# Performance work log

Hardware: AMD Instinct MI355X
Metric: run time of the kernel (lower is better)

Reference implementation:

```python
import jax, jax.numpy as jnp
import numpy as np

EPS = 0.5
GAM1 = 1.0
GAM2 = 1.0
GAM3 = 1.0


def setup_inputs() -> dict:
    key = jax.random.key(0)
    k1, k2, k3 = jax.random.split(key, 3)
    n, d, C = 8192, 512, 10
    Z = jax.random.normal(k1, (n, d), dtype=jnp.float32)
    Z_bar = jax.random.normal(k2, (n, d), dtype=jnp.float32)
    real_label = jax.random.randint(k3, (n,), 0, C)
    return {"Z": Z, "Z_bar": Z_bar, "real_label": real_label, "num_classes": C}


def _mcr_terms(Z, Z_bar, real_label, num_classes):
    n, d = Z.shape
    dtype = Z.dtype
    Pi = jax.nn.one_hot(real_label, num_classes, dtype=dtype)  # [n, C]
    counts = Pi.sum(axis=0)                                    # [C]
    I = jnp.eye(d, dtype=dtype)

    # Discriminative terms: logdet(I + d/(n*eps) * Z^T Z) / 2
    disc_z = jnp.linalg.slogdet(I + (d / (n * EPS)) * (Z.T @ Z))[1] / 2.0
    disc_zb = jnp.linalg.slogdet(I + (d / (n * EPS)) * (Z_bar.T @ Z_bar))[1] / 2.0

    # Per-class Grams: Z[:, mask_j] @ Z[:, mask_j].T == Z^T diag(Pi[:,j]) Z
    Gz = jnp.einsum('nc,nd,ne->cde', Pi, Z, Z)          # [C, d, d]
    Gzb = jnp.einsum('nc,nd,ne->cde', Pi, Z_bar, Z_bar)  # [C, d, d]

    trPi = counts + 1e-8                                 # matches torch's +1e-08
    scal = (d / (trPi * EPS))[:, None, None]
    ld_z = jnp.linalg.slogdet(I[None] + scal * Gz)[1]    # raw logdets (not halved)
    ld_zb = jnp.linalg.slogdet(I[None] + scal * Gzb)[1]
    s = trPi / (2.0 * n)
    comp_z = jnp.sum(s * ld_z)
    comp_zb = jnp.sum(s * ld_zb)

    z_total = -(disc_z - comp_z)
    zb_total = -(disc_zb - comp_zb)

    # R(z_j, zbar_j): concat rows -> Gram sum, n_j = 2*count_j (exact count)
    n_j = 2.0 * counts
    scal3 = (d / (n_j * EPS))[:, None, None]
    ld3 = jnp.linalg.slogdet(I[None] + scal3 * (Gz + Gzb))[1] / 2.0
    item = jnp.sum(ld3)

    term3 = item - 0.25 * jnp.sum(ld_z) - 0.25 * jnp.sum(ld_zb)
    errD = -(GAM1 * (disc_z - comp_z) + GAM2 * (disc_zb - comp_zb) + GAM3 * term3)
    return errD, z_total, zb_total, term3


def reference(Z, Z_bar, real_label, num_classes):
    errD, z_total, zb_total, term3 = _mcr_terms(Z, Z_bar, real_label, num_classes)
    # empi = [z_total, zbar_total, term3]; pack everything into one vector
    return jnp.stack([errD, z_total, zb_total, term3])
```

## Files before the change

kernel.cpp:

```cpp
#include <hip/hip_runtime.h>
#include <math.h>

#define NROWS 8192
#define DIM   512
#define NCLS  10
#define GT    4
#define GPAIR 10
#define NMAT  32

typedef __attribute__((ext_vector_type(8))) short bf16x8;
typedef __attribute__((ext_vector_type(4))) float f32x4;

__device__ __forceinline__ float rdlane(float v, int l) {
    return __int_as_float(__builtin_amdgcn_readlane(__float_as_int(v), l));
}

__device__ __forceinline__ void fact64(float (*Dl)[68], float* dinv, float* ldm, int lane) {
    float row_[64];
    #pragma unroll
    for (int j = 0; j < 64; ++j) row_[j] = Dl[lane][j];
    float dval = 1.f;
    #pragma unroll
    for (int k = 0; k < 64; ++k) {
        float piv = rdlane(row_[k], k);
        float s = 1.0f / sqrtf(piv);
        float lik = row_[k] * s;
        dval = (lane == k) ? lik : dval;
        row_[k] = lik;
        #pragma unroll
        for (int j = k + 1; j < 64; ++j)
            row_[j] -= lik * rdlane(lik, j);
    }
    #pragma unroll
    for (int j = 0; j < 64; ++j) Dl[lane][j] = row_[j];
    dinv[lane] = 1.f / dval;
    float v = 2.f * logf(dval);
    #pragma unroll
    for (int off = 32; off > 0; off >>= 1) v += __shfl_down(v, off);
    if (lane == 0) atomicAdd(ldm, v);
}

__global__ __launch_bounds__(256) void k_count(const int* __restrict__ label,
                                               int* __restrict__ counts,
                                               int* __restrict__ lists) {
    __shared__ int hist[NCLS];
    __shared__ int base[NCLS];
    __shared__ int lofs[NCLS];
    int tid = threadIdx.x;
    int i = blockIdx.x * 256 + tid;
    if (tid < NCLS) { hist[tid] = 0; lofs[tid] = 0; }
    __syncthreads();
    int c = label[i];
    atomicAdd(&hist[c], 1);
    __syncthreads();
    if (tid < NCLS) base[tid] = atomicAdd(&counts[tid], hist[tid]);
    __syncthreads();
    int lpos = atomicAdd(&lofs[c], 1);
    lists[(size_t)c * NROWS + base[c] + lpos] = i;
}

__global__ __launch_bounds__(512) void k_gram(const float* __restrict__ Z,
                                              const float* __restrict__ Zb,
                                              const int* __restrict__ counts,
                                              const int* __restrict__ lists,
                                              float* __restrict__ G) {
    int pt = blockIdx.x;
    int c  = blockIdx.y;
    int tz = blockIdx.z;
    int ti = 0, tj = 0;
    { int p = pt;
      for (int r = 0; r < GT; ++r) { if (p <= r) { ti = r; tj = p; break; } p -= (r + 1); } }
    bool diag = (ti == tj);

    const float* __restrict__ src = tz ? Zb : Z;
    float* __restrict__ Gout = G + (((size_t)tz * NCLS + c) * GPAIR + pt) * 16384;
    int cnt = counts[c];
    const int* __restrict__ list = lists + (size_t)c * NROWS;

    __shared__ float As[2][32][132];
    __shared__ float Bs[2][32][132];
    int tid = threadIdx.x;
    int gid = tid >> 8;
    int t   = tid & 255;
    int tx = t & 15, ty = t >> 4;
    int sr = t >> 3, se = t & 7;

    float acc[8][8];
    #pragma unroll
    for (int r = 0; r < 8; ++r)
        #pragma unroll
        for (int s = 0; s < 8; ++s) acc[r][s] = 0.f;

    float4 pa[4], pb[4];
    {
        int gr = gid * 32 + sr;
        #pragma unroll
        for (int q = 0; q < 4; ++q) { pa[q] = make_float4(0.f,0.f,0.f,0.f); pb[q] = pa[q]; }
        if (gr < cnt) {
            const float* __restrict__ rp = src + (size_t)list[gr] * DIM;
            #pragma unroll
            for (int q = 0; q < 4; ++q) {
                pa[q] = *(const float4*)&rp[ti * 128 + se * 16 + q * 4];
                if (!diag) pb[q] = *(const float4*)&rp[tj * 128 + se * 16 + q * 4];
            }
        }
    }

    for (int base0 = 0; base0 < cnt; base0 += 64) {
        #pragma unroll
        for (int q = 0; q < 4; ++q) {
            *(float4*)&As[gid][sr][se * 16 + q * 4] = pa[q];
            if (!diag) *(float4*)&Bs[gid][sr][se * 16 + q * 4] = pb[q];
        }
        __syncthreads();
        {
            int gr = base0 + 64 + gid * 32 + sr;
            #pragma unroll
            for (int q = 0; q < 4; ++q) { pa[q] = make_float4(0.f,0.f,0.f,0.f); pb[q] = pa[q]; }
            if (gr < cnt) {
                const float* __restrict__ rp = src + (size_t)list[gr] * DIM;
                #pragma unroll
                for (int q = 0; q < 4; ++q) {
                    pa[q] = *(const float4*)&rp[ti * 128 + se * 16 + q * 4];
                    if (!diag) pb[q] = *(const float4*)&rp[tj * 128 + se * 16 + q * 4];
                }
            }
        }
        const float (*__restrict__ Ap)[132] = As[gid];
        const float (*__restrict__ Bp)[132] = diag ? As[gid] : Bs[gid];
        #pragma unroll
        for (int kk = 0; kk < 32; ++kk) {
            float a[8], b[8];
            *(float4*)&a[0] = *(const float4*)&Ap[kk][ty * 4];
            *(float4*)&a[4] = *(const float4*)&Ap[kk][64 + ty * 4];
            *(float4*)&b[0] = *(const float4*)&Bp[kk][tx * 4];
            *(float4*)&b[4] = *(const float4*)&Bp[kk][64 + tx * 4];
            #pragma unroll
            for (int r = 0; r < 8; ++r)
                #pragma unroll
                for (int s = 0; s < 8; ++s)
                    acc[r][s] += a[r] * b[s];
        }
        __syncthreads();
    }

    float* red = (float*)&As[0][0][0];
    #pragma unroll
    for (int r = 0; r < 8; ++r) {
        __syncthreads();
        if (gid == 1) {
            #pragma unroll
            for (int s = 0; s < 8; ++s) red[t * 8 + s] = acc[r][s];
        }
        __syncthreads();
        if (gid == 0) {
            #pragma unroll
            for (int s = 0; s < 8; ++s) acc[r][s] += red[t * 8 + s];
        }
    }
    if (gid == 0) {
        #pragma unroll
        for (int r = 0; r < 8; ++r) {
            int row = (r < 4) ? (ty * 4 + r) : (64 + ty * 4 + r - 4);
            float4 v0 = make_float4(acc[r][0], acc[r][1], acc[r][2], acc[r][3]);
            float4 v1 = make_float4(acc[r][4], acc[r][5], acc[r][6], acc[r][7]);
            *(float4*)&Gout[(size_t)row * 128 + tx * 4]      = v0;
            *(float4*)&Gout[(size_t)row * 128 + 64 + tx * 4] = v1;
        }
    }
}

__global__ __launch_bounds__(256) void k_assemble(const float* __restrict__ G,
                                                  const int* __restrict__ counts,
                                                  float* __restrict__ A) {
    int pt = blockIdx.x;
    int m  = blockIdx.y;
    int ti = 0, tj = 0;
    { int p = pt;
      for (int r = 0; r < GT; ++r) { if (p <= r) { ti = r; tj = p; break; } p -= (r + 1); } }

    const size_t TILE = 16384;
    const float* __restrict__ Gz  = G;
    const float* __restrict__ Gzb = G + (size_t)NCLS * GPAIR * TILE;
    float* __restrict__ Am = A + (size_t)m * DIM * DIM;
    int tid = threadIdx.x;

    int mode; int c; float sc;
    if (m < 10)      { mode = 0; c = m;      sc = 1024.f / ((float)counts[c] + 1e-8f); }
    else if (m < 20) { mode = 1; c = m - 10; sc = 1024.f / ((float)counts[c] + 1e-8f); }
    else if (m < 30) { mode = 2; c = m - 20; sc = 512.f / (float)counts[c]; }
    else             { mode = (m == 30) ? 3 : 4; c = 0; sc = 0.125f; }

    #pragma unroll 1
    for (int h = 0; h < 16; ++h) {
        int id = h * 256 + tid;
        int row = id >> 5, c4 = id & 31;
        size_t off = (size_t)row * 128 + c4 * 4;
        float4 g = make_float4(0.f, 0.f, 0.f, 0.f);
        if (mode == 0) {
            g = *(const float4*)&Gz[((size_t)c * GPAIR + pt) * TILE + off];
        } else if (mode == 1) {
            g = *(const float4*)&Gzb[((size_t)c * GPAIR + pt) * TILE + off];
        } else if (mode == 2) {
            float4 a = *(const float4*)&Gz [((size_t)c * GPAIR + pt) * TILE + off];
            float4 b = *(const float4*)&Gzb[((size_t)c * GPAIR + pt) * TILE + off];
            g.x = a.x + b.x; g.y = a.y + b.y; g.z = a.z + b.z; g.w = a.w + b.w;
        } else if (mode == 3) {
            for (int cc = 0; cc < NCLS; ++cc) {
                float4 t = *(const float4*)&Gz[((size_t)cc * GPAIR + pt) * TILE + off];
                g.x += t.x; g.y += t.y; g.z += t.z; g.w += t.w;
            }
        } else {
            for (int cc = 0; cc < NCLS; ++cc) {
                float4 t = *(const float4*)&Gzb[((size_t)cc * GPAIR + pt) * TILE + off];
                g.x += t.x; g.y += t.y; g.z += t.z; g.w += t.w;
            }
        }
        g.x *= sc; g.y *= sc; g.z *= sc; g.w *= sc;
        if (ti == tj) {
            int cb = c4 * 4;
            if (row == cb)     g.x += 1.f;
            if (row == cb + 1) g.y += 1.f;
            if (row == cb + 2) g.z += 1.f;
            if (row == cb + 3) g.w += 1.f;
        }
        *(float4*)&Am[(size_t)(ti * 128 + row) * DIM + tj * 128 + c4 * 4] = g;
    }
}

__global__ __launch_bounds__(512, 2) void k_chol(float* __restrict__ A,
                                                 float* __restrict__ ld) {
    int m = blockIdx.x;
    float* __restrict__ Am = A + (size_t)m * DIM * DIM;
    int tid = threadIdx.x;
    int wave = tid >> 6, lane = tid & 63;

    __shared__ float  Dl[64][68];
    __shared__ float  dinv[64];
    __shared__ ushort Thi[448][64];
    __shared__ ushort Tlo[448][64];

    for (int h = tid; h < 1024; h += 512) {
        int r = h >> 4, c4 = h & 15;
        *(float4*)&Dl[r][c4 * 4] = *(const float4*)&Am[(size_t)r * DIM + c4 * 4];
    }
    __syncthreads();
    if (wave == 0) fact64(Dl, dinv, &ld[m], lane);
    __syncthreads();

    #pragma unroll 1
    for (int p = 0; p < 7; ++p) {
        int col0 = p * 64, col1 = col0 + 64;
        int mt = DIM - col1;
        int K = mt >> 6;
        int npair = K * (K + 1) / 2;

        int chunk = wave - 1;
        if (chunk >= 0 && chunk < K) {
            float Lreg[64];
            #pragma unroll
            for (int j4 = 0; j4 < 16; ++j4)
                *(float4*)&Lreg[j4 * 4] = *(const float4*)&Dl[lane][j4 * 4];
            float dv = dinv[lane];
            const float* __restrict__ Brow = Am + (size_t)(col1 + chunk * 64 + lane) * DIM + col0;
            float t[64];
            float4 bv;
            #pragma unroll
            for (int i = 0; i < 64; ++i) {
                if ((i & 3) == 0) bv = *(const float4*)&Brow[i];
                float a0 = (i & 3) == 0 ? bv.x : ((i & 3) == 1 ? bv.y : ((i & 3) == 2 ? bv.z : bv.w));
                float a1 = 0.f, a2 = 0.f, a3 = 0.f;
                int mm = 0;
                #pragma unroll
                for (; mm + 3 < i; mm += 4) {
                    a0 -= t[mm]     * rdlane(Lreg[mm],     i);
                    a1 -= t[mm + 1] * rdlane(Lreg[mm + 1], i);
                    a2 -= t[mm + 2] * rdlane(Lreg[mm + 2], i);
                    a3 -= t[mm + 3] * rdlane(Lreg[mm + 3], i);
                }
                #pragma unroll
                for (; mm < i; ++mm) a0 -= t[mm] * rdlane(Lreg[mm], i);
                t[i] = ((a0 + a1) + (a2 + a3)) * rdlane(dv, i);
            }
            int row = chunk * 64 + lane;
            int hsw = (row & 7) << 3;
            #pragma unroll
            for (int i = 0; i < 64; i += 2) {
                uint u0 = __float_as_uint(t[i]);
                float h0f = __uint_as_float(u0 & 0xFFFF0000u);
                uint l0 = __float_as_uint(t[i] - h0f);
                uint u1 = __float_as_uint(t[i + 1]);
                float h1f = __uint_as_float(u1 & 0xFFFF0000u);
                uint l1 = __float_as_uint(t[i + 1] - h1f);
                int idx = i ^ hsw;
                *(uint*)&Thi[row][idx] = (u0 >> 16) | (u1 & 0xFFFF0000u);
                *(uint*)&Tlo[row][idx] = (l0 >> 16) | (l1 & 0xFFFF0000u);
            }
        }
        __syncthreads();

        int lr = lane & 15, kb = lane >> 4;
        if (wave == 0) {
            f32x4 acc[4][4];
            #pragma unroll
            for (int it = 0; it < 4; ++it)
                #pragma unroll
                for (int jt = 0; jt < 4; ++jt)
                    acc[it][jt] = (f32x4){0.f, 0.f, 0.f, 0.f};
            #pragma unroll
            for (int k0 = 0; k0 < 64; k0 += 32) {
                bf16x8 Ah[4], Al[4];
                int idx = (k0 + kb * 8) ^ ((lr & 7) << 3);
                #pragma unroll
                for (int it = 0; it < 4; ++it) {
                    int rowA = it * 16 + lr;
                    Ah[it] = *(const bf16x8*)&Thi[rowA][idx];
                    Al[it] = *(const bf16x8*)&Tlo[rowA][idx];
                }
                #pragma unroll
                for (int it = 0; it < 4; ++it)
                    #pragma unroll
                    for (int jt = 0; jt < 4; ++jt) {
                        acc[it][jt] = __builtin_amdgcn_mfma_f32_16x16x32_bf16(Ah[it], Ah[jt], acc[it][jt], 0, 0, 0);
                        acc[it][jt] = __builtin_amdgcn_mfma_f32_16x16x32_bf16(Ah[it], Al[jt], acc[it][jt], 0, 0, 0);
                        acc[it][jt] = __builtin_amdgcn_mfma_f32_16x16x32_bf16(Al[it], Ah[jt], acc[it][jt], 0, 0, 0);
                    }
            }
            #pragma unroll
            for (int it = 0; it < 4; ++it)
                #pragma unroll
                for (int jt = 0; jt < 4; ++jt)
                    #pragma unroll
                    for (int rg = 0; rg < 4; ++rg) {
                        int r = it * 16 + kb * 4 + rg;
                        int cg = jt * 16 + lr;
                        float orig = Am[(size_t)(col1 + r) * DIM + col1 + cg];
                        Dl[r][cg] = orig - acc[it][jt][rg];
                    }
            fact64(Dl, dinv, &ld[m], lane);
        } else {
            for (int tix = wave; tix < npair; tix += 7) {
                int a = 0, b = 0;
                { int q = tix;
                  for (int r0 = 0; r0 < 7; ++r0) { if (q <= r0) { a = r0; b = q; break; } q -= (r0 + 1); } }
                f32x4 acc[4][4];
                #pragma unroll
                for (int it = 0; it < 4; ++it)
                    #pragma unroll
                    for (int jt = 0; jt < 4; ++jt)
                        acc[it][jt] = (f32x4){0.f, 0.f, 0.f, 0.f};
                #pragma unroll
                for (int k0 = 0; k0 < 64; k0 += 32) {
                    bf16x8 Ah[4], Al[4], Bh[4], Bl[4];
                    int idx = (k0 + kb * 8) ^ ((lr & 7) << 3);
                    #pragma unroll
                    for (int it = 0; it < 4; ++it) {
                        int rowA = a * 64 + it * 16 + lr;
                        Ah[it] = *(const bf16x8*)&Thi[rowA][idx];
                        Al[it] = *(const bf16x8*)&Tlo[rowA][idx];
                        int rowB = b * 64 + it * 16 + lr;
                        Bh[it] = *(const bf16x8*)&Thi[rowB][idx];
                        Bl[it] = *(const bf16x8*)&Tlo[rowB][idx];
                    }
                    #pragma unroll
                    for (int it = 0; it < 4; ++it)
                        #pragma unroll
                        for (int jt = 0; jt < 4; ++jt) {
                            acc[it][jt] = __builtin_amdgcn_mfma_f32_16x16x32_bf16(Ah[it], Bh[jt], acc[it][jt], 0, 0, 0);
                            acc[it][jt] = __builtin_amdgcn_mfma_f32_16x16x32_bf16(Ah[it], Bl[jt], acc[it][jt], 0, 0, 0);
                            acc[it][jt] = __builtin_amdgcn_mfma_f32_16x16x32_bf16(Al[it], Bh[jt], acc[it][jt], 0, 0, 0);
                        }
                }
                #pragma unroll
                for (int it = 0; it < 4; ++it)
                    #pragma unroll
                    for (int jt = 0; jt < 4; ++jt)
                        #pragma unroll
                        for (int rg = 0; rg < 4; ++rg) {
                            int gi = col1 + a * 64 + it * 16 + kb * 4 + rg;
                            int gj = col1 + b * 64 + jt * 16 + lr;
                            Am[(size_t)gi * DIM + gj] -= acc[it][jt][rg];
                        }
            }
        }
        __syncthreads();
    }
}

__global__ void k_final(const float* __restrict__ ld,
                        const int* __restrict__ counts,
                        float* __restrict__ out) {
    if (threadIdx.x == 0 && blockIdx.x == 0) {
        float disc_z  = 0.5f * ld[30];
        float disc_zb = 0.5f * ld[31];
        float comp_z = 0.f, comp_zb = 0.f, sum_ldz = 0.f, sum_ldzb = 0.f, item = 0.f;
        for (int c = 0; c < NCLS; ++c) {
            float trPi = (float)counts[c] + 1e-8f;
            float s = trPi / (2.f * (float)NROWS);
            comp_z  += s * ld[c];
            comp_zb += s * ld[10 + c];
            sum_ldz  += ld[c];
            sum_ldzb += ld[10 + c];
            item += 0.5f * ld[20 + c];
        }
        float term3 = item - 0.25f * sum_ldz - 0.25f * sum_ldzb;
        float z_total  = -(disc_z - comp_z);
        float zb_total = -(disc_zb - comp_zb);
        float errD = -((disc_z - comp_z) + (disc_zb - comp_zb) + term3);
        out[0] = errD; out[1] = z_total; out[2] = zb_total; out[3] = term3;
    }
}

extern "C" void kernel_launch(void* const* d_in, const int* in_sizes, int n_in,
                              void* d_out, int out_size, void* d_ws, size_t ws_size,
                              hipStream_t stream) {
    (void)in_sizes; (void)n_in; (void)out_size; (void)ws_size;
    const float* Z     = (const float*)d_in[0];
    const float* Zb    = (const float*)d_in[1];
    const int*   label = (const int*)d_in[2];

    char* ws = (char*)d_ws;
    int*   counts = (int*)ws;
    float* ld     = (float*)(ws + 64);
    int*   lists  = (int*)(ws + 256);
    float* G      = (float*)(ws + 256 + (size_t)NCLS * NROWS * 4);
    float* A      = G + (size_t)2 * NCLS * GPAIR * 16384;
    float* out    = (float*)d_out;

    hipMemsetAsync(ws, 0, 256, stream);
    k_count<<<NROWS / 256, 256, 0, stream>>>(label, counts, lists);
    k_gram<<<dim3(GPAIR, NCLS, 2), 512, 0, stream>>>(Z, Zb, counts, lists, G);
    k_assemble<<<dim3(GPAIR, NMAT), 256, 0, stream>>>(G, counts, A);
    k_chol<<<NMAT, 512, 0, stream>>>(A, ld);
    k_final<<<1, 64, 0, stream>>>(ld, counts, out);
}
```

Baseline: 509.0 us.

## Compute per-class Gram tiles with split-bf16 MFMA instead of FP32 FMA

Rewrites the per-class Gram kernel to use 16x16x32 bf16 MFMA instructions. Each fp32 value is split into a bf16 hi part and a bf16 lo residual, and three MFMAs (hi*hi, hi*lo, lo*hi) approximate fp32 accuracy. Shared memory is laid out transposed with an XOR swizzle to avoid bank conflicts. The two-group cross-block reduction and the register prefetch are removed, and the global loads become scalar gathers. The aim is to cut the FP32 FMA cost of the Gram computation, at some loss of precision and load efficiency.

```diff
diff --git a/kernel.cpp b/kernel.cpp
--- a/kernel.cpp
+++ b/kernel.cpp
@@ -77,97 +77,75 @@
     int cnt = counts[c];
     const int* __restrict__ list = lists + (size_t)c * NROWS;
 
-    __shared__ float As[2][32][132];
-    __shared__ float Bs[2][32][132];
-    int tid = threadIdx.x;
-    int gid = tid >> 8;
-    int t   = tid & 255;
-    int tx = t & 15, ty = t >> 4;
-    int sr = t >> 3, se = t & 7;
-
-    float acc[8][8];
-    #pragma unroll
-    for (int r = 0; r < 8; ++r)
+    __shared__ __align__(16) ushort Ahi[128][64];
+    __shared__ __align__(16) ushort Alo[128][64];
+    __shared__ __align__(16) ushort Bhi[128][64];
+    __shared__ __align__(16) ushort Blo[128][64];
+
+    int tid = threadIdx.x, wave = tid >> 6, lane = tid & 63;
+    int lr = lane & 15, kb = lane >> 4;
+
+    f32x4 acc[8];
+    #pragma unroll
+    for (int jt = 0; jt < 8; ++jt) acc[jt] = (f32x4){0.f, 0.f, 0.f, 0.f};
+
+    int upw = diag ? 8 : 16;
+
+    for (int base0 = 0; base0 < cnt; base0 += 64) {
+        #pragma unroll 1
+        for (int q = 0; q < upw; ++q) {
+            int u  = wave * upw + q;
+            int op = (u >> 6) & 1;
+            int cs = (u >> 5) & 1;
+            int kp = u & 31;
+            int col = cs * 64 + lane;
+            int tcol = (op ? tj : ti) * 128 + col;
+            int g0 = base0 + 2 * kp, g1 = g0 + 1;
+            float v0 = 0.f, v1 = 0.f;
+            if (g0 < cnt) v0 = src[(size_t)list[g0] * DIM + tcol];
+            if (g1 < cnt) v1 = src[(size_t)list[g1] * DIM + tcol];
+            uint h0 = __float_as_uint(v0) & 0xFFFF0000u;
+            uint h1 = __float_as_uint(v1) & 0xFFFF0000u;
+            uint l0 = __float_as_uint(v0 - __uint_as_float(h0));
+            uint l1 = __float_as_uint(v1 - __uint_as_float(h1));
+            int kidx = (2 * kp) ^ ((lane & 7) << 3);
+            uint hv = (h0 >> 16) | h1;
+            uint lv = (l0 >> 16) | (l1 & 0xFFFF0000u);
+            if (op == 0) {
+                *(uint*)&Ahi[col][kidx] = hv;
+                *(uint*)&Alo[col][kidx] = lv;
+            } else {
+                *(uint*)&Bhi[col][kidx] = hv;
+                *(uint*)&Blo[col][kidx] = lv;
+            }
+        }
+        __syncthreads();
+
+        const ushort (*__restrict__ BH)[64] = diag ? Ahi : Bhi;
+        const ushort (*__restrict__ BL)[64] = diag ? Alo : Blo;
+        int swz = (lr & 7) << 3;
         #pragma unroll
-        for (int s = 0; s < 8; ++s) acc[r][s] = 0.f;
-
-    float4 pa[4], pb[4];
-    {
-        int gr = gid * 32 + sr;
+        for (int k0 = 0; k0 < 64; k0 += 32) {
+            int kidx = (k0 + kb * 8) ^ swz;
+            bf16x8 aH = *(const bf16x8*)&Ahi[wave * 16 + lr][kidx];
+            bf16x8 aL = *(const bf16x8*)&Alo[wave * 16 + lr][kidx];
+            #pragma unroll
+            for (int jt = 0; jt < 8; ++jt) {
+                bf16x8 bH = *(const bf16x8*)&BH[jt * 16 + lr][kidx];
+                bf16x8 bL = *(const bf16x8*)&BL[jt * 16 + lr][kidx];
+                acc[jt] = __builtin_amdgcn_mfma_f32_16x16x32_bf16(aH, bH, acc[jt], 0, 0, 0);
+                acc[jt] = __builtin_amdgcn_mfma_f32_16x16x32_bf16(aH, bL, acc[jt], 0, 0, 0);
+                acc[jt] = __builtin_amdgcn_mfma_f32_16x16x32_bf16(aL, bH, acc[jt], 0, 0, 0);
+            }
+        }
+        __syncthreads();
+    }
+
+    #pragma unroll
+    for (int jt = 0; jt < 8; ++jt)
         #pragma unroll
-        for (int q = 0; q < 4; ++q) { pa[q] = make_float4(0.f,0.f,0.f,0.f); pb[q] = pa[q]; }
-        if (gr < cnt) {
-            const float* __restrict__ rp = src + (size_t)list[gr] * DIM;
-            #pragma unroll
-            for (int q = 0; q < 4; ++q) {
-                pa[q] = *(const float4*)&rp[ti * 128 + se * 16 + q * 4];
-                if (!diag) pb[q] = *(const float4*)&rp[tj * 128 + se * 16 + q * 4];
-            }
-        }
-    }
-
-    for (int base0 = 0; base0 < cnt; base0 += 64) {
-        #pragma unroll
-        for (int q = 0; q < 4; ++q) {
-            *(float4*)&As[gid][sr][se * 16 + q * 4] = pa[q];
-            if (!diag) *(float4*)&Bs[gid][sr][se * 16 + q * 4] = pb[q];
-        }
-        __syncthreads();
-        {
-            int gr = base0 + 64 + gid * 32 + sr;
-            #pragma unroll
-            for (int q = 0; q < 4; ++q) { pa[q] = make_float4(0.f,0.f,0.f,0.f); pb[q] = pa[q]; }
-            if (gr < cnt) {
-                const float* __restrict__ rp = src + (size_t)list[gr] * DIM;
-                #pragma unroll
-                for (int q = 0; q < 4; ++q) {
-                    pa[q] = *(const float4*)&rp[ti * 128 + se * 16 + q * 4];
-                    if (!diag) pb[q] = *(const float4*)&rp[tj * 128 + se * 16 + q * 4];
-                }
-            }
-        }
-        const float (*__restrict__ Ap)[132] = As[gid];
-        const float (*__restrict__ Bp)[132] = diag ? As[gid] : Bs[gid];
-        #pragma unroll
-        for (int kk = 0; kk < 32; ++kk) {
-            float a[8], b[8];
-            *(float4*)&a[0] = *(const float4*)&Ap[kk][ty * 4];
-            *(float4*)&a[4] = *(const float4*)&Ap[kk][64 + ty * 4];
-            *(float4*)&b[0] = *(const float4*)&Bp[kk][tx * 4];
-            *(float4*)&b[4] = *(const float4*)&Bp[kk][64 + tx * 4];
-            #pragma unroll
-            for (int r = 0; r < 8; ++r)
-                #pragma unroll
-                for (int s = 0; s < 8; ++s)
-                    acc[r][s] += a[r] * b[s];
-        }
-        __syncthreads();
-    }
-
-    float* red = (float*)&As[0][0][0];
-    #pragma unroll
-    for (int r = 0; r < 8; ++r) {
-        __syncthreads();
-        if (gid == 1) {
-            #pragma unroll
-            for (int s = 0; s < 8; ++s) red[t * 8 + s] = acc[r][s];
-        }
-        __syncthreads();
-        if (gid == 0) {
-            #pragma unroll
-            for (int s = 0; s < 8; ++s) acc[r][s] += red[t * 8 + s];
-        }
-    }
-    if (gid == 0) {
-        #pragma unroll
-        for (int r = 0; r < 8; ++r) {
-            int row = (r < 4) ? (ty * 4 + r) : (64 + ty * 4 + r - 4);
-            float4 v0 = make_float4(acc[r][0], acc[r][1], acc[r][2], acc[r][3]);
-            float4 v1 = make_float4(acc[r][4], acc[r][5], acc[r][6], acc[r][7]);
-            *(float4*)&Gout[(size_t)row * 128 + tx * 4]      = v0;
-            *(float4*)&Gout[(size_t)row * 128 + 64 + tx * 4] = v1;
-        }
-    }
+        for (int rg = 0; rg < 4; ++rg)
+            Gout[(size_t)(wave * 16 + kb * 4 + rg) * 128 + jt * 16 + lr] = acc[jt][rg];
 }
 
 __global__ __launch_bounds__(256) void k_assemble(const float* __restrict__ G,
```

After: 621.6 us. 1.22x slower.
